# Performance work log

Hardware: AMD Instinct MI355X
Metric: run time of the kernel (lower is better)

## Reference

```python
import jax, jax.numpy as jnp
import numpy as np
from jax import lax

G, BS = 8, 32  # group_num, blocksize


def conv(x, w, b=None, stride=1, pad=0):
    out = lax.conv_general_dilated(x, w, (stride, stride), [(pad, pad), (pad, pad)],
                                   dimension_numbers=('NCHW', 'OIHW', 'NCHW'))
    if b is not None:
        out = out + b[None, :, None, None]
    return out


def prelu(x, a):
    return jnp.where(x >= 0, x, a * x)


def reshape_adap(x, bs):
    # faithful vectorized form of My_Reshape_Adap: channel c = co*bs*bs + p*bs + q
    # goes to output[b, co, i*bs+p, j*bs+q]
    B, C, h, w = x.shape
    co = C // (bs * bs)
    return x.reshape(B, co, bs, bs, h, w).transpose(0, 1, 4, 2, 5, 3).reshape(B, co, h * bs, w * bs)


def setup_inputs() -> dict:
    key = jax.random.key(0)
    ks = jax.random.split(key, 24)
    rn = lambda k, shp, s: (jax.random.normal(k, shp, dtype=jnp.float32) * s)
    inp = {
        'x': rn(ks[0], (1, 1, 256, 256), 1.0),
        'sample_w': rn(ks[1], (G, 13, 1, 32, 32), 0.03),
        'up_w': rn(ks[2], (G, 1024, 13, 1, 1), 0.2),
        'up_b': rn(ks[3], (G, 1024), 0.02),
        'h1_w': rn(ks[4], (G, 64, 1, 3, 3), 0.2),
        'h1_b': rn(ks[5], (G, 64), 0.02),
        'h1_a': jnp.full((G,), 0.25, jnp.float32),
        'fus_w': rn(ks[6], (G - 1, 64, 128, 3, 3), 0.03),
        'fus_b': rn(ks[7], (G - 1, 64), 0.02),
        'fus_a': jnp.full((G - 1,), 0.25, jnp.float32),
        't2_w': rn(ks[8], (G, 64, 64, 3, 3), 0.04),
        't2_b': rn(ks[9], (G, 64), 0.02),
        't2_a': jnp.full((G,), 0.25, jnp.float32),
        't3_w': rn(ks[10], (G, 64, 64, 3, 3), 0.04),
        't3_b': rn(ks[11], (G, 64), 0.02),
        't3_a': jnp.full((G,), 0.25, jnp.float32),
        't4_w': rn(ks[12], (G, 64, 64, 3, 3), 0.04),
        't4_b': rn(ks[13], (G, 64), 0.02),
        't4_a': jnp.full((G,), 0.25, jnp.float32),
        't5_w': rn(ks[14], (G, 1, 64, 3, 3), 0.04),
        't5_b': rn(ks[15], (G, 1), 0.02),
    }
    return inp


def reference(x, sample_w, up_w, up_b, h1_w, h1_b, h1_a, fus_w, fus_b, fus_a,
              t2_w, t2_b, t2_a, t3_w, t3_b, t3_a, t4_w, t4_b, t4_a, t5_w, t5_b):
    outs = []
    feature = None
    for m in range(G):
        # SamplingModule: conv(1->13, k=32, s=32, no bias)
        s = conv(x, sample_w[m], stride=BS)
        # HeadBlock: 1x1 upsample (13->1024) + block scatter reshape + conv(1->64)+PReLU
        u = conv(s, up_w[m], up_b[m])
        r = reshape_adap(u, BS)                       # [B,1,H,W]
        h = prelu(conv(r, h1_w[m], h1_b[m], pad=1), h1_a[m])  # [B,64,H,W]
        if m == 0:
            feature = h
        else:
            # Fusion_concate: conv(128->64)+PReLU on channel concat
            cat = jnp.concatenate([feature, h], axis=1)
            feature = prelu(conv(cat, fus_w[m - 1], fus_b[m - 1], pad=1), fus_a[m - 1])
        t = prelu(conv(feature, t2_w[m], t2_b[m], pad=1), t2_a[m])
        t = prelu(conv(t, t3_w[m], t3_b[m], pad=1), t3_a[m])
        t = prelu(conv(t, t4_w[m], t4_b[m], pad=1), t4_a[m])
        outs.append(conv(t, t5_w[m], t5_b[m], pad=1))
    return jnp.stack(outs)  # [G, B, 1, H, W]
```

## Files before the change

kernel.cpp:

```cpp
#include <hip/hip_runtime.h>

constexpr int H = 256, W = 256, NPIX = H * W;
constexpr int PW = 258;
constexpr size_t PLANE = (size_t)PW * PW * 64;

typedef _Float16 half8 __attribute__((ext_vector_type(8)));
typedef _Float16 half4 __attribute__((ext_vector_type(4)));
typedef float    f32x4 __attribute__((ext_vector_type(4)));
typedef float    f32x16 __attribute__((ext_vector_type(16)));

__device__ __forceinline__ void gl16(const _Float16* g, _Float16* l)
{
    __builtin_amdgcn_global_load_lds(
        (const __attribute__((address_space(1))) unsigned int*)g,
        (__attribute__((address_space(3))) unsigned int*)l, 16, 0, 0);
}

__global__ __launch_bounds__(256)
void border_k(_Float16* __restrict__ planes)
{
    int tid = blockIdx.x * 256 + threadIdx.x;
    if (tid >= 24 * 1028 * 8) return;
    int c = tid & 7, rem = tid >> 3;
    int p = rem / 1028, b = rem % 1028;
    int gy, gx;
    if (b < 258)      { gy = 0;           gx = b; }
    else if (b < 516) { gy = 257;         gx = b - 258; }
    else if (b < 772) { gy = b - 516 + 1; gx = 0; }
    else              { gy = b - 772 + 1; gx = 257; }
    f32x4 z = {0.f, 0.f, 0.f, 0.f};
    *(f32x4*)(planes + (size_t)p * PLANE + ((size_t)(gy * PW + gx) * 64) + c * 8) = z;
}

__global__ __launch_bounds__(256)
void sampup_k(const float* __restrict__ x, const float* __restrict__ sw,
              const float* __restrict__ uw, const float* __restrict__ ub,
              float* __restrict__ r_all)
{
    int m = blockIdx.x >> 6, ij = blockIdx.x & 63;
    int i = ij >> 3, j = ij & 7;
    __shared__ float s_lds[16];
    int t = threadIdx.x;
    if (t < 208) {
        int c = t >> 4, sub = t & 15;
        float acc = 0.f;
        for (int k = sub * 64; k < sub * 64 + 64; ++k) {
            int p = k >> 5, q = k & 31;
            acc += x[(i * 32 + p) * W + (j * 32 + q)] * sw[(m * 13 + c) * 1024 + k];
        }
        #pragma unroll
        for (int off = 8; off; off >>= 1) acc += __shfl_down(acc, off, 16);
        if (sub == 0) s_lds[c] = acc;
    }
    __syncthreads();
    const float* uwm = uw + m * 1024 * 13;
    float* rm = r_all + m * NPIX;
    #pragma unroll
    for (int pi = 0; pi < 4; ++pi) {
        int px = pi * 256 + t;
        int p = px >> 5, q = px & 31;
        int oc = p * 32 + q;
        float acc = ub[m * 1024 + oc];
        #pragma unroll
        for (int c = 0; c < 13; ++c) acc = fmaf(uwm[oc * 13 + c], s_lds[c], acc);
        rm[((i * 32 + p) << 8) + j * 32 + q] = acc;
    }
}

__global__ __launch_bounds__(256)
void h1_k(const float* __restrict__ r_all, const float* __restrict__ w,
          const float* __restrict__ b, const float* __restrict__ a,
          _Float16* __restrict__ f0)
{
    const float* r = r_all;
    const int t = threadIdx.x;
    const int px = t & 63, cog = t >> 6;
    const int y = blockIdx.x >> 2;
    const int x = ((blockIdx.x & 3) << 6) + px;
    float v[9];
    #pragma unroll
    for (int dy = 0; dy < 3; ++dy) {
        int gy = y + dy - 1;
        #pragma unroll
        for (int dx = 0; dx < 3; ++dx) {
            int gx = x + dx - 1;
            v[dy*3+dx] = ((unsigned)gy < 256u && (unsigned)gx < 256u)
                       ? r[(gy << 8) + gx] : 0.f;
        }
    }
    const float slope = a[0];
    _Float16* op = f0 + ((size_t)((y + 1) * PW + (x + 1))) * 64 + cog * 16;
    #pragma unroll
    for (int cg2 = 0; cg2 < 2; ++cg2) {
        half8 o;
        #pragma unroll
        for (int j = 0; j < 8; ++j) {
            int co = cog * 16 + cg2 * 8 + j;
            float acc = b[co];
            #pragma unroll
            for (int k = 0; k < 9; ++k) acc = fmaf(v[k], w[co*9+k], acc);
            acc = acc >= 0.f ? acc : slope * acc;
            o[j] = (_Float16)acc;
        }
        *(half8*)(op + cg2 * 8) = o;
    }
}

__global__ __launch_bounds__(256)
void wprep_k(const float* __restrict__ t2w, const float* __restrict__ t3w,
             const float* __restrict__ t4w, const float* __restrict__ fusw,
             _Float16* __restrict__ w16)
{
    int tid = blockIdx.x * 256 + threadIdx.x;
    if (tid >= 38 * 36864) return;
    int blk = tid / 36864, r2 = tid % 36864;
    int e = r2 & 7, co = (r2 >> 3) & 63, hh = (r2 >> 9) & 1, kk = (r2 >> 10) & 3,
        tap = r2 >> 12;
    const float* src; int cin, cib;
    if (blk < 24) {
        int which = blk >> 3, m = blk & 7;
        src = (which == 0 ? t2w : which == 1 ? t3w : t4w) + (size_t)m * 64 * 64 * 9;
        cin = 64; cib = 0;
    } else {
        int f = (blk - 24) >> 1; cib = ((blk - 24) & 1) * 64;
        src = fusw + (size_t)f * 64 * 128 * 9; cin = 128;
    }
    int ci = cib + (kk * 2 + hh) * 8 + e;
    w16[tid] = (_Float16)src[((size_t)co * cin + ci) * 9 + tap];
}

__global__ __launch_bounds__(256, 2)
void conv_mfma_k(const _Float16* __restrict__ in0, const _Float16* __restrict__ w0,
                 const float* __restrict__ bias, const float* __restrict__ alpha,
                 _Float16* __restrict__ out)
{
    const int t    = threadIdx.x;
    const int lane = t & 63;
    const int wv   = t >> 6;
    const int b    = blockIdx.x;
    const int m    = b >> 6;
    const int rem  = b & 63;
    const int xh   = rem & 1;
    const int y0   = (rem >> 1) << 3;

    const _Float16* inp0 = in0 + (size_t)m * PLANE;
    _Float16*       outp = out + (size_t)m * PLANE;
    const _Float16* wp0  = w0 + (size_t)m * 36864;
    const float*    bp   = bias + m * 64;
    const float     slope = alpha[m];
    const int x0 = xh << 7;

    const int h = lane >> 5, cl = lane & 31;
    const int cohalf = wv >> 1, px0 = (wv & 1) * 64, cobase = cohalf * 32;

    extern __shared__ __align__(16) char smem[];
    _Float16* li = (_Float16*)smem;

    half8 Areg[36];
    #pragma unroll
    for (int tap = 0; tap < 9; ++tap)
        #pragma unroll
        for (int kk = 0; kk < 4; ++kk)
            Areg[tap*4+kk] = *(const half8*)(wp0 +
                (size_t)(((tap*4+kk)*2 + h)*64 + cobase + cl) * 8);

    auto stage_row = [&](int pr) {
        const int slot = pr & 3;
        #pragma unroll
        for (int i = 0; i < 5; ++i) {
            int f = i * 256 + t;
            if (i < 4 || f < 1040) {
                int hx = f >> 3, c = f & 7;
                gl16(inp0 + ((size_t)(pr * PW + x0 + hx) * 64 + (c ^ (hx & 7)) * 8),
                     li + (size_t)(slot * 1040 + f) * 8);
            }
        }
    };

    f32x16 acc0, acc1;

    stage_row(y0); stage_row(y0 + 1); stage_row(y0 + 2);
    __syncthreads();
    #pragma unroll 1
    for (int s = 0; s < 8; ++s) {
        if (s < 7) stage_row(y0 + s + 3);
        #pragma unroll
        for (int q = 0; q < 4; ++q)
            #pragma unroll
            for (int j = 0; j < 4; ++j) {
                float bb = bp[cobase + q * 8 + 4 * h + j];
                acc0[q*4+j] = bb; acc1[q*4+j] = bb;
            }
        __builtin_amdgcn_s_setprio(1);
        #pragma unroll
        for (int tap = 0; tap < 9; ++tap) {
            const int dy = tap / 3, dx = tap % 3;
            const int slot = (y0 + s + dy) & 3;
            const int hx0 = px0 + cl + dx;
            const int hx1 = hx0 + 32;
            const int sw8 = hx0 & 7;
            #pragma unroll
            for (int kk = 0; kk < 4; ++kk) {
                const int c = kk * 2 + h;
                half8 b0 = *(const half8*)(li + ((size_t)((slot*130 + hx0)*8 + (c ^ sw8))) * 8);
                half8 b1 = *(const half8*)(li + ((size_t)((slot*130 + hx1)*8 + (c ^ sw8))) * 8);
                acc0 = __builtin_amdgcn_mfma_f32_32x32x16_f16(Areg[tap*4+kk], b0, acc0, 0, 0, 0);
                acc1 = __builtin_amdgcn_mfma_f32_32x32x16_f16(Areg[tap*4+kk], b1, acc1, 0, 0, 0);
            }
        }
        __builtin_amdgcn_s_setprio(0);
        const int y = y0 + s;
        #pragma unroll
        for (int pt = 0; pt < 2; ++pt) {
            const size_t gp = (size_t)((y + 1) * PW + (x0 + px0 + pt * 32 + cl + 1)) * 64;
            const f32x16& A0 = pt ? acc1 : acc0;
            #pragma unroll
            for (int q = 0; q < 4; ++q) {
                half4 v0;
                #pragma unroll
                for (int j = 0; j < 4; ++j) {
                    float xv = A0[q*4+j];
                    xv = xv >= 0.f ? xv : slope * xv;
                    v0[j] = (_Float16)xv;
                }
                *(half4*)(outp + gp + cobase + q * 8 + 4 * h) = v0;
            }
        }
        if (s < 7) {
            asm volatile("s_waitcnt vmcnt(8)" ::: "memory");
            __builtin_amdgcn_s_barrier();
            __builtin_amdgcn_sched_barrier(0);
        }
    }
}

__global__ __launch_bounds__(256, 2)
void fus_k(const _Float16* __restrict__ fprev, const float* __restrict__ rm,
           const float* __restrict__ h1w, const float* __restrict__ h1b,
           const float* __restrict__ h1a,
           const _Float16* __restrict__ wf, const _Float16* __restrict__ wh,
           const float* __restrict__ bias, const float* __restrict__ alpha,
           _Float16* __restrict__ outp)
{
    const int t = threadIdx.x, lane = t & 63, wv = t >> 6;
    const int b = blockIdx.x;
    const int xcd = b & 7, u = b >> 3, xq = u & 3, band = u >> 2;
    const int y0 = xcd * 32 + band * 2, x0 = xq * 64;
    const int h = lane >> 5, cl = lane & 31;
    const int px0 = (wv & 1) * 32, cobase = (wv >> 1) * 32;

    __shared__ __align__(16) _Float16 ringF[4 * 528 * 8];
    __shared__ __align__(16) _Float16 ringH[4 * 528 * 8];

    #pragma unroll
    for (int i = 0; i < 9; ++i) {
        int idx = i * 256 + t;
        if (i < 8 || idx < 2112) {
            int r = idx / 528, f = idx - r * 528;
            int hx = f >> 3, c = f & 7;
            gl16(fprev + ((size_t)((y0 + r) * PW + x0 + hx) * 64 + (c ^ (hx & 7)) * 8),
                 ringF + (size_t)idx * 8);
        }
    }

    {
        const int c8 = t & 7;
        float wreg[72];
        #pragma unroll
        for (int i = 0; i < 18; ++i)
            *(f32x4*)(wreg + i * 4) = *(const f32x4*)(h1w + c8 * 72 + i * 4);
        float b8[8];
        #pragma unroll
        for (int j = 0; j < 8; ++j) b8[j] = h1b[c8 * 8 + j];
        const float hs = h1a[0];

        #pragma unroll
        for (int it = 0; it < 9; ++it) {
            int idx = it * 256 + t;
            if (it < 8 || idx < 2112) {
                int pl = idx >> 3;
                int r  = pl / 66, hx = pl - r * 66;
                int gy = y0 - 1 + r, gx = x0 - 1 + hx;
                half8 o = {0,0,0,0,0,0,0,0};
                if ((unsigned)gy < 256u && (unsigned)gx < 256u) {
                    float v[9];
                    #pragma unroll
                    for (int dy = 0; dy < 3; ++dy) {
                        int ry = gy + dy - 1;
                        #pragma unroll
                        for (int dx = 0; dx < 3; ++dx) {
                            int rx = gx + dx - 1;
                            v[dy*3+dx] = ((unsigned)ry < 256u && (unsigned)rx < 256u)
                                       ? rm[(ry << 8) + rx] : 0.f;
                        }
                    }
                    #pragma unroll
                    for (int j = 0; j < 8; ++j) {
                        float a = b8[j];
                        #pragma unroll
                        for (int k = 0; k < 9; ++k) a = fmaf(v[k], wreg[j*9+k], a);
                        a = a >= 0.f ? a : hs * a;
                        o[j] = (_Float16)a;
                    }
                }
                *(half8*)(ringH + (size_t)(r * 528 + hx * 8 + (c8 ^ (hx & 7))) * 8) = o;
            }
        }
    }
    __builtin_amdgcn_sched_barrier(0);

    half8 Areg[36];
    auto load_A = [&](const _Float16* w) {
        #pragma unroll
        for (int tap = 0; tap < 9; ++tap)
            #pragma unroll
            for (int kk = 0; kk < 4; ++kk)
                Areg[tap*4+kk] = *(const half8*)(w +
                    (size_t)(((tap*4+kk)*2 + h)*64 + cobase + cl) * 8);
    };
    load_A(wf);

    f32x16 acc0, acc1;
    #pragma unroll
    for (int q = 0; q < 4; ++q)
        #pragma unroll
        for (int j = 0; j < 4; ++j) {
            float bb = bias[cobase + q * 8 + 4 * h + j];
            acc0[q*4+j] = bb; acc1[q*4+j] = bb;
        }

    __syncthreads();

    auto cpass = [&](const _Float16* ring) {
        __builtin_amdgcn_s_setprio(1);
        #pragma unroll
        for (int tap = 0; tap < 9; ++tap) {
            const int dy = tap / 3, dx = tap % 3;
            const int hx = px0 + cl + dx;
            const int sw = hx & 7;
            #pragma unroll
            for (int kk = 0; kk < 4; ++kk) {
                const int c = kk * 2 + h;
                half8 b0 = *(const half8*)(ring + ((size_t)(((dy    )*528) + hx*8 + (c ^ sw))) * 8);
                half8 b1 = *(const half8*)(ring + ((size_t)(((dy + 1)*528) + hx*8 + (c ^ sw))) * 8);
                acc0 = __builtin_amdgcn_mfma_f32_32x32x16_f16(Areg[tap*4+kk], b0, acc0, 0, 0, 0);
                acc1 = __builtin_amdgcn_mfma_f32_32x32x16_f16(Areg[tap*4+kk], b1, acc1, 0, 0, 0);
            }
        }
        __builtin_amdgcn_s_setprio(0);
    };

    cpass(ringF);
    load_A(wh);
    cpass(ringH);

    const float slope = alpha[0];
    #pragma unroll
    for (int s = 0; s < 2; ++s) {
        const size_t gp = (size_t)((y0 + s + 1) * PW + (x0 + px0 + cl + 1)) * 64 + cobase;
        const f32x16& A0 = s ? acc1 : acc0;
        #pragma unroll
        for (int q = 0; q < 4; ++q) {
            half4 v;
            #pragma unroll
            for (int j = 0; j < 4; ++j) {
                float xv = A0[q*4+j];
                xv = xv >= 0.f ? xv : slope * xv;
                v[j] = (_Float16)xv;
            }
            *(half4*)(outp + gp + q * 8 + 4 * h) = v;
        }
    }
}

__global__ __launch_bounds__(256, 2)
void t5_k(const _Float16* __restrict__ in_all, const float* __restrict__ w_all,
          const float* __restrict__ b_all, float* __restrict__ out_all)
{
    const int m = blockIdx.y;
    const _Float16* in = in_all + (size_t)m * PLANE;
    const float* w = w_all + m * 576;
    float* outp = out_all + m * NPIX;

    const int t = threadIdx.x;
    const int b = blockIdx.x;
    const int xcd = b & 7, u = b >> 3;
    const int xh = u & 1, band = u >> 1;
    const int y0 = xcd * 32 + band * 8;
    const int x0 = xh << 7;

    __shared__ __align__(16) _Float16 ring[4 * 130 * 64];
    __shared__ float wl[576];
    __shared__ float part[128];

    auto stage_row = [&](int pr) {
        const int slot = pr & 3;
        #pragma unroll
        for (int i = 0; i < 5; ++i) {
            int f = i * 256 + t;
            if (i < 4 || f < 1040) {
                int hx = f >> 3, c = f & 7;
                gl16(in + ((size_t)(pr * PW + x0 + hx) * 64 + (c ^ (hx & 7)) * 8),
                     ring + (size_t)(slot * 1040 + f) * 8);
            }
        }
    };

    stage_row(y0); stage_row(y0 + 1); stage_row(y0 + 2);
    #pragma unroll
    for (int i = 0; i < 3; ++i) { int idx = i*256 + t; if (idx < 576) wl[idx] = w[idx]; }
    __syncthreads();

    const int p = t & 127, chalf = t >> 7;
    #pragma unroll 1
    for (int s = 0; s < 8; ++s) {
        if (s < 7) stage_row(y0 + s + 3);
        float acc = 0.f;
        #pragma unroll
        for (int dy = 0; dy < 3; ++dy) {
            const int slot = (y0 + s + dy) & 3;
            #pragma unroll
            for (int dx = 0; dx < 3; ++dx) {
                const int hx = p + dx, sw = hx & 7, tap = dy * 3 + dx;
                #pragma unroll
                for (int kc = 0; kc < 4; ++kc) {
                    const int c8 = chalf * 4 + kc;
                    half8 vv = *(const half8*)(ring +
                        ((size_t)((slot*130 + hx)*8 + (c8 ^ sw))) * 8);
                    #pragma unroll
                    for (int e = 0; e < 8; ++e)
                        acc = fmaf((float)vv[e], wl[(c8 * 8 + e) * 9 + tap], acc);
                }
            }
        }
        if (chalf) part[p] = acc;
        __syncthreads();
        if (!chalf) outp[((y0 + s) << 8) + x0 + p] = part[p] + acc + b_all[m];
        __syncthreads();
    }
}

extern "C" void kernel_launch(void* const* d_in, const int* in_sizes, int n_in,
                              void* d_out, int out_size, void* d_ws, size_t ws_size,
                              hipStream_t stream)
{
    const float* x        = (const float*)d_in[0];
    const float* sample_w = (const float*)d_in[1];
    const float* up_w     = (const float*)d_in[2];
    const float* up_b     = (const float*)d_in[3];
    const float* h1_w     = (const float*)d_in[4];
    const float* h1_b     = (const float*)d_in[5];
    const float* h1_a     = (const float*)d_in[6];
    const float* fus_w    = (const float*)d_in[7];
    const float* fus_b    = (const float*)d_in[8];
    const float* fus_a    = (const float*)d_in[9];
    const float* t2_w     = (const float*)d_in[10];
    const float* t2_b     = (const float*)d_in[11];
    const float* t2_a     = (const float*)d_in[12];
    const float* t3_w     = (const float*)d_in[13];
    const float* t3_b     = (const float*)d_in[14];
    const float* t3_a     = (const float*)d_in[15];
    const float* t4_w     = (const float*)d_in[16];
    const float* t4_b     = (const float*)d_in[17];
    const float* t4_a     = (const float*)d_in[18];
    const float* t5_w     = (const float*)d_in[19];
    const float* t5_b     = (const float*)d_in[20];

    float* out = (float*)d_out;
    char*  wsb = (char*)d_ws;

    _Float16* w16    = (_Float16*)wsb;
    float*    r_all  = (float*)(wsb + 2801664);
    _Float16* f_all  = (_Float16*)(wsb + 4898816);
    _Float16* sc_all = f_all + 8 * PLANE;
    _Float16* t1_all = sc_all + 8 * PLANE;

    auto wblk = [&](int b) { return w16 + (size_t)b * 36864; };

    border_k<<<771, 256, 0, stream>>>(f_all);
    wprep_k<<<5472, 256, 0, stream>>>(t2_w, t3_w, t4_w, fus_w, w16);
    sampup_k<<<512, 256, 0, stream>>>(x, sample_w, up_w, up_b, r_all);
    h1_k<<<1024, 256, 0, stream>>>(r_all, h1_w, h1_b, h1_a, f_all);

    for (int m = 1; m < 8; ++m) {
        fus_k<<<512, 256, 0, stream>>>(
            f_all + (size_t)(m - 1) * PLANE,
            r_all + m * NPIX, h1_w + m * 576, h1_b + m * 64, h1_a + m,
            wblk(24 + (m - 1) * 2), wblk(24 + (m - 1) * 2 + 1),
            fus_b + (m - 1) * 64, fus_a + (m - 1),
            f_all + (size_t)m * PLANE);
    }

    const size_t LDSB = 66560;
    conv_mfma_k<<<512, 256, LDSB, stream>>>(f_all, wblk(0), t2_b, t2_a, t1_all);
    conv_mfma_k<<<512, 256, LDSB, stream>>>(t1_all, wblk(8), t3_b, t3_a, sc_all);
    conv_mfma_k<<<512, 256, LDSB, stream>>>(sc_all, wblk(16), t4_b, t4_a, t1_all);
    t5_k<<<dim3(64, 8), 256, 0, stream>>>(t1_all, t5_w, t5_b, out);
}
```

Baseline: 390.5 us.

## Merge prep kernels and shrink conv tiles to 64-wide with 128-thread blocks

Three setup kernels (border zeroing, weight conversion, sampling/upsample) are merged into one launch using grid-stride loops, which removes two launch overheads. The tail conv kernel now uses 128-thread blocks, each covering a 64-pixel-wide strip with two waves splitting the output channels. This doubles the grid to 1024 blocks and halves LDS use per block, aiming for more blocks in flight and better CU balance. In exchange, each block loads a proportionally larger halo and keeps its own copy of the weight registers.

```diff
diff --git a/kernel.cpp b/kernel.cpp
--- a/kernel.cpp
+++ b/kernel.cpp
@@ -17,53 +17,69 @@
 }
 
 __global__ __launch_bounds__(256)
-void border_k(_Float16* __restrict__ planes)
-{
-    int tid = blockIdx.x * 256 + threadIdx.x;
-    if (tid >= 24 * 1028 * 8) return;
-    int c = tid & 7, rem = tid >> 3;
-    int p = rem / 1028, b = rem % 1028;
-    int gy, gx;
-    if (b < 258)      { gy = 0;           gx = b; }
-    else if (b < 516) { gy = 257;         gx = b - 258; }
-    else if (b < 772) { gy = b - 516 + 1; gx = 0; }
-    else              { gy = b - 772 + 1; gx = 257; }
-    f32x4 z = {0.f, 0.f, 0.f, 0.f};
-    *(f32x4*)(planes + (size_t)p * PLANE + ((size_t)(gy * PW + gx) * 64) + c * 8) = z;
-}
-
-__global__ __launch_bounds__(256)
-void sampup_k(const float* __restrict__ x, const float* __restrict__ sw,
-              const float* __restrict__ uw, const float* __restrict__ ub,
-              float* __restrict__ r_all)
-{
-    int m = blockIdx.x >> 6, ij = blockIdx.x & 63;
-    int i = ij >> 3, j = ij & 7;
-    __shared__ float s_lds[16];
-    int t = threadIdx.x;
-    if (t < 208) {
-        int c = t >> 4, sub = t & 15;
-        float acc = 0.f;
-        for (int k = sub * 64; k < sub * 64 + 64; ++k) {
-            int p = k >> 5, q = k & 31;
-            acc += x[(i * 32 + p) * W + (j * 32 + q)] * sw[(m * 13 + c) * 1024 + k];
-        }
-        #pragma unroll
-        for (int off = 8; off; off >>= 1) acc += __shfl_down(acc, off, 16);
-        if (sub == 0) s_lds[c] = acc;
-    }
-    __syncthreads();
-    const float* uwm = uw + m * 1024 * 13;
-    float* rm = r_all + m * NPIX;
-    #pragma unroll
-    for (int pi = 0; pi < 4; ++pi) {
-        int px = pi * 256 + t;
-        int p = px >> 5, q = px & 31;
-        int oc = p * 32 + q;
-        float acc = ub[m * 1024 + oc];
-        #pragma unroll
-        for (int c = 0; c < 13; ++c) acc = fmaf(uwm[oc * 13 + c], s_lds[c], acc);
-        rm[((i * 32 + p) << 8) + j * 32 + q] = acc;
+void prep_k(const float* __restrict__ x, const float* __restrict__ sw,
+            const float* __restrict__ uw, const float* __restrict__ ub,
+            const float* __restrict__ t2w, const float* __restrict__ t3w,
+            const float* __restrict__ t4w, const float* __restrict__ fusw,
+            _Float16* __restrict__ planes, _Float16* __restrict__ w16,
+            float* __restrict__ r_all)
+{
+    const int b = blockIdx.x, t = threadIdx.x;
+    for (int idx = b * 256 + t; idx < 24 * 1028 * 8; idx += 512 * 256) {
+        int c = idx & 7, rem = idx >> 3;
+        int p = rem / 1028, bb = rem % 1028;
+        int gy, gx;
+        if (bb < 258)      { gy = 0;            gx = bb; }
+        else if (bb < 516) { gy = 257;          gx = bb - 258; }
+        else if (bb < 772) { gy = bb - 516 + 1; gx = 0; }
+        else               { gy = bb - 772 + 1; gx = 257; }
+        f32x4 z = {0.f, 0.f, 0.f, 0.f};
+        *(f32x4*)(planes + (size_t)p * PLANE + ((size_t)(gy * PW + gx) * 64) + c * 8) = z;
+    }
+    for (int idx = b * 256 + t; idx < 38 * 36864; idx += 512 * 256) {
+        int blk = idx / 36864, r2 = idx % 36864;
+        int e = r2 & 7, co = (r2 >> 3) & 63, hh = (r2 >> 9) & 1, kk = (r2 >> 10) & 3,
+            tap = r2 >> 12;
+        const float* src; int cin, cib;
+        if (blk < 24) {
+            int which = blk >> 3, m = blk & 7;
+            src = (which == 0 ? t2w : which == 1 ? t3w : t4w) + (size_t)m * 64 * 64 * 9;
+            cin = 64; cib = 0;
+        } else {
+            int f = (blk - 24) >> 1; cib = ((blk - 24) & 1) * 64;
+            src = fusw + (size_t)f * 64 * 128 * 9; cin = 128;
+        }
+        int ci = cib + (kk * 2 + hh) * 8 + e;
+        w16[idx] = (_Float16)src[((size_t)co * cin + ci) * 9 + tap];
+    }
+    {
+        int m = b >> 6, ij = b & 63;
+        int i = ij >> 3, j = ij & 7;
+        __shared__ float s_lds[16];
+        if (t < 208) {
+            int c = t >> 4, sub = t & 15;
+            float acc = 0.f;
+            for (int k = sub * 64; k < sub * 64 + 64; ++k) {
+                int p = k >> 5, q = k & 31;
+                acc += x[(i * 32 + p) * W + (j * 32 + q)] * sw[(m * 13 + c) * 1024 + k];
+            }
+            #pragma unroll
+            for (int off = 8; off; off >>= 1) acc += __shfl_down(acc, off, 16);
+            if (sub == 0) s_lds[c] = acc;
+        }
+        __syncthreads();
+        const float* uwm = uw + m * 1024 * 13;
+        float* rm = r_all + m * NPIX;
+        #pragma unroll
+        for (int pi = 0; pi < 4; ++pi) {
+            int px = pi * 256 + t;
+            int p = px >> 5, q = px & 31;
+            int oc = p * 32 + q;
+            float acc = ub[m * 1024 + oc];
+            #pragma unroll
+            for (int c = 0; c < 13; ++c) acc = fmaf(uwm[oc * 13 + c], s_lds[c], acc);
+            rm[((i * 32 + p) << 8) + j * 32 + q] = acc;
+        }
     }
 }
 
@@ -106,30 +122,7 @@
     }
 }
 
-__global__ __launch_bounds__(256)
-void wprep_k(const float* __restrict__ t2w, const float* __restrict__ t3w,
-             const float* __restrict__ t4w, const float* __restrict__ fusw,
-             _Float16* __restrict__ w16)
-{
-    int tid = blockIdx.x * 256 + threadIdx.x;
-    if (tid >= 38 * 36864) return;
-    int blk = tid / 36864, r2 = tid % 36864;
-    int e = r2 & 7, co = (r2 >> 3) & 63, hh = (r2 >> 9) & 1, kk = (r2 >> 10) & 3,
-        tap = r2 >> 12;
-    const float* src; int cin, cib;
-    if (blk < 24) {
-        int which = blk >> 3, m = blk & 7;
-        src = (which == 0 ? t2w : which == 1 ? t3w : t4w) + (size_t)m * 64 * 64 * 9;
-        cin = 64; cib = 0;
-    } else {
-        int f = (blk - 24) >> 1; cib = ((blk - 24) & 1) * 64;
-        src = fusw + (size_t)f * 64 * 128 * 9; cin = 128;
-    }
-    int ci = cib + (kk * 2 + hh) * 8 + e;
-    w16[tid] = (_Float16)src[((size_t)co * cin + ci) * 9 + tap];
-}
-
-__global__ __launch_bounds__(256, 2)
+__global__ __launch_bounds__(128, 2)
 void conv_mfma_k(const _Float16* __restrict__ in0, const _Float16* __restrict__ w0,
                  const float* __restrict__ bias, const float* __restrict__ alpha,
                  _Float16* __restrict__ out)
@@ -138,20 +131,20 @@
     const int lane = t & 63;
     const int wv   = t >> 6;
     const int b    = blockIdx.x;
-    const int m    = b >> 6;
-    const int rem  = b & 63;
-    const int xh   = rem & 1;
-    const int y0   = (rem >> 1) << 3;
+    const int m    = b >> 7;
+    const int rem  = b & 127;
+    const int xq   = rem & 3;
+    const int y0   = (rem >> 2) << 3;
+    const int x0   = xq << 6;
 
     const _Float16* inp0 = in0 + (size_t)m * PLANE;
     _Float16*       outp = out + (size_t)m * PLANE;
     const _Float16* wp0  = w0 + (size_t)m * 36864;
     const float*    bp   = bias + m * 64;
     const float     slope = alpha[m];
-    const int x0 = xh << 7;
 
     const int h = lane >> 5, cl = lane & 31;
-    const int cohalf = wv >> 1, px0 = (wv & 1) * 64, cobase = cohalf * 32;
+    const int cobase = wv * 32;
 
     extern __shared__ __align__(16) char smem[];
     _Float16* li = (_Float16*)smem;
@@ -168,11 +161,11 @@
         const int slot = pr & 3;
         #pragma unroll
         for (int i = 0; i < 5; ++i) {
-            int f = i * 256 + t;
-            if (i < 4 || f < 1040) {
+            int f = i * 128 + t;
+            if (i < 4 || f < 528) {
                 int hx = f >> 3, c = f & 7;
                 gl16(inp0 + ((size_t)(pr * PW + x0 + hx) * 64 + (c ^ (hx & 7)) * 8),
-                     li + (size_t)(slot * 1040 + f) * 8);
+                     li + (size_t)(slot * 528 + f) * 8);
             }
         }
     };
@@ -196,14 +189,14 @@
         for (int tap = 0; tap < 9; ++tap) {
             const int dy = tap / 3, dx = tap % 3;
             const int slot = (y0 + s + dy) & 3;
-            const int hx0 = px0 + cl + dx;
+            const int hx0 = cl + dx;
             const int hx1 = hx0 + 32;
             const int sw8 = hx0 & 7;
             #pragma unroll
             for (int kk = 0; kk < 4; ++kk) {
                 const int c = kk * 2 + h;
-                half8 b0 = *(const half8*)(li + ((size_t)((slot*130 + hx0)*8 + (c ^ sw8))) * 8);
-                half8 b1 = *(const half8*)(li + ((size_t)((slot*130 + hx1)*8 + (c ^ sw8))) * 8);
+                half8 b0 = *(const half8*)(li + ((size_t)(slot*528 + hx0*8 + (c ^ sw8))) * 8);
+                half8 b1 = *(const half8*)(li + ((size_t)(slot*528 + hx1*8 + (c ^ sw8))) * 8);
                 acc0 = __builtin_amdgcn_mfma_f32_32x32x16_f16(Areg[tap*4+kk], b0, acc0, 0, 0, 0);
                 acc1 = __builtin_amdgcn_mfma_f32_32x32x16_f16(Areg[tap*4+kk], b1, acc1, 0, 0, 0);
             }
@@ -212,7 +205,7 @@
         const int y = y0 + s;
         #pragma unroll
         for (int pt = 0; pt < 2; ++pt) {
-            const size_t gp = (size_t)((y + 1) * PW + (x0 + px0 + pt * 32 + cl + 1)) * 64;
+            const size_t gp = (size_t)((y + 1) * PW + (x0 + pt * 32 + cl + 1)) * 64;
             const f32x16& A0 = pt ? acc1 : acc0;
             #pragma unroll
             for (int q = 0; q < 4; ++q) {
@@ -221,6 +214,7 @@
                 for (int j = 0; j < 4; ++j) {
                     float xv = A0[q*4+j];
                     xv = xv >= 0.f ? xv : slope * xv;
+                    v0[j] = (_Float16)v0[j];
                     v0[j] = (_Float16)xv;
                 }
                 *(half4*)(outp + gp + cobase + q * 8 + 4 * h) = v0;
@@ -262,7 +256,6 @@
                  ringF + (size_t)idx * 8);
         }
     }
-
     {
         const int c8 = t & 7;
         float wreg[72];
@@ -296,11 +289,11 @@
                     }
                     #pragma unroll
                     for (int j = 0; j < 8; ++j) {
-                        float a = b8[j];
+                        float av = b8[j];
                         #pragma unroll
-                        for (int k = 0; k < 9; ++k) a = fmaf(v[k], wreg[j*9+k], a);
-                        a = a >= 0.f ? a : hs * a;
-                        o[j] = (_Float16)a;
+                        for (int k = 0; k < 9; ++k) av = fmaf(v[k], wreg[j*9+k], av);
+                        av = av >= 0.f ? av : hs * av;
+                        o[j] = (_Float16)av;
                     }
                 }
                 *(half8*)(ringH + (size_t)(r * 528 + hx * 8 + (c8 ^ (hx & 7))) * 8) = o;
@@ -477,9 +470,9 @@
 
     auto wblk = [&](int b) { return w16 + (size_t)b * 36864; };
 
-    border_k<<<771, 256, 0, stream>>>(f_all);
-    wprep_k<<<5472, 256, 0, stream>>>(t2_w, t3_w, t4_w, fus_w, w16);
-    sampup_k<<<512, 256, 0, stream>>>(x, sample_w, up_w, up_b, r_all);
+    prep_k<<<512, 256, 0, stream>>>(x, sample_w, up_w, up_b,
+                                    t2_w, t3_w, t4_w, fus_w,
+                                    f_all, w16, r_all);
     h1_k<<<1024, 256, 0, stream>>>(r_all, h1_w, h1_b, h1_a, f_all);
 
     for (int m = 1; m < 8; ++m) {
@@ -491,9 +484,9 @@
             f_all + (size_t)m * PLANE);
     }
 
-    const size_t LDSB = 66560;
-    conv_mfma_k<<<512, 256, LDSB, stream>>>(f_all, wblk(0), t2_b, t2_a, t1_all);
-    conv_mfma_k<<<512, 256, LDSB, stream>>>(t1_all, wblk(8), t3_b, t3_a, sc_all);
-    conv_mfma_k<<<512, 256, LDSB, stream>>>(sc_all, wblk(16), t4_b, t4_a, t1_all);
+    const size_t LDSB = 33792;
+    conv_mfma_k<<<1024, 128, LDSB, stream>>>(f_all, wblk(0), t2_b, t2_a, t1_all);
+    conv_mfma_k<<<1024, 128, LDSB, stream>>>(t1_all, wblk(8), t3_b, t3_a, sc_all);
+    conv_mfma_k<<<1024, 128, LDSB, stream>>>(sc_all, wblk(16), t4_b, t4_a, t1_all);
     t5_k<<<dim3(64, 8), 256, 0, stream>>>(t1_all, t5_w, t5_b, out);
 }
```

Result: no change. 393.2 us (+0.7%).
